# Kernel optimization log

Hardware: AMD Instinct MI355X
Metric: run time of the kernel (lower is better)

Reference implementation:

```python
import jax, jax.numpy as jnp
import numpy as np


def _reduce1(x):
    # x: [B, n, d] -> [B, 2d]; exists=max, forall=min over objects (exclude_self is a no-op for cnt=1)
    return jnp.concatenate([x.max(axis=1), x.min(axis=1)], axis=-1)


def _reduce2(x):
    # x: [B, n, n, d] -> [B, n, 2d]; exclude_self masks diagonal i==j (0 for exists/max, 1 for forall/min)
    n = x.shape[1]
    diag = jnp.eye(n, dtype=bool)[None, :, :, None]
    exists = jnp.where(diag, 0.0, x).max(axis=2)
    forall = jnp.where(diag, 1.0, x).min(axis=2)
    return jnp.concatenate([exists, forall], axis=-1)


def _layer(f0, f1, f2, p):
    # One LogicLayer step (breadth=2, minmax reducer, exclude_self, sigmoid norm, no hidden layers)
    W0, b0, W1, b1, W2, b2 = p
    B, n, d1 = f1.shape
    # order 0: [self, reduce(order1)]
    g0 = jnp.concatenate([f0, _reduce1(f1)], axis=-1)
    o0 = jax.nn.sigmoid(g0 @ W0 + b0)
    # order 1: [expand(order0), self, reduce(order2)]
    e0 = jnp.broadcast_to(f0[:, None, :], (B, n, f0.shape[-1]))
    g1 = jnp.concatenate([e0, f1, _reduce2(f2)], axis=-1)
    o1 = jax.nn.sigmoid(g1 @ W1 + b1)
    # order 2: [expand(order1), self] then Permutation(2) = cat(x, swap(i,j))
    e1 = jnp.broadcast_to(f1[:, :, None, :], (B, n, n, d1))
    g2 = jnp.concatenate([e1, f2], axis=-1)
    g2 = jnp.concatenate([g2, jnp.swapaxes(g2, 1, 2)], axis=-1)
    o2 = jax.nn.sigmoid(g2 @ W2 + b2)
    return o0, o1, o2


def setup_inputs() -> dict:
    key = jax.random.key(0)
    B, n = 4, 256
    d = [32, 64, 64]
    O = 128
    ks = iter(jax.random.split(key, 64))
    inp = {
        "x0": jax.random.uniform(next(ks), (B, d[0]), dtype=jnp.float32),
        "x1": jax.random.uniform(next(ks), (B, n, d[1]), dtype=jnp.float32),
        "x2": jax.random.uniform(next(ks), (B, n, n, d[2]), dtype=jnp.float32),
    }
    fan_ins = [
        (d[0] + 2 * d[1], d[0] + d[1] + 2 * d[2], 2 * (d[1] + d[2])),  # layer 0
        (O + 2 * O, O + O + 2 * O, 2 * (O + O)),                        # layer 1
        (O + 2 * O, O + O + 2 * O, 2 * (O + O)),                        # layer 2
    ]
    for l, fins in enumerate(fan_ins):
        for o, fin in enumerate(fins):
            inp[f"W{o}_{l}"] = jax.random.normal(next(ks), (fin, O), dtype=jnp.float32) / np.sqrt(fin).astype(np.float32)
            inp[f"b{o}_{l}"] = jnp.zeros((O,), dtype=jnp.float32)
    return inp


def reference(x0, x1, x2,
              W0_0, b0_0, W1_0, b1_0, W2_0, b2_0,
              W0_1, b0_1, W1_1, b1_1, W2_1, b2_1,
              W0_2, b0_2, W1_2, b1_2, W2_2, b2_2):
    f = (x0, x1, x2)
    for p in ((W0_0, b0_0, W1_0, b1_0, W2_0, b2_0),
              (W0_1, b0_1, W1_1, b1_1, W2_1, b2_1),
              (W0_2, b0_2, W1_2, b1_2, W2_2, b2_2)):
        f = _layer(*f, p)
    return f
```

## Files before the change

kernel.cpp:

```cpp
#include <hip/hip_runtime.h>
#include <hip/hip_bf16.h>
#include <cstdint>

#define NN 256
#define NB 4
#define OC 128

using bf16x8_t = __attribute__((ext_vector_type(8))) __bf16;
using f32x4_t  = __attribute__((ext_vector_type(4))) float;

typedef const __attribute__((address_space(1))) uint8_t* gptr1_t;
typedef __attribute__((address_space(3))) uint8_t* lptr3_t;

__device__ __forceinline__ void async_load16(const void* g, void* l) {
  __builtin_amdgcn_global_load_lds((gptr1_t)g, (lptr3_t)l, 16, 0, 0);
}

__device__ __forceinline__ float sigf(float x) {
  return __builtin_amdgcn_rcpf(1.0f + __expf(-x));
}

__device__ __forceinline__ uint16_t f2bf_rne(float f) {
  uint32_t u = __float_as_uint(f);
  uint32_t r = (u + 0x7fffu + ((u >> 16) & 1u)) >> 16;
  return (uint16_t)r;
}

__device__ __forceinline__ void emit_wt(const float* __restrict__ W2,
                                        uint16_t* __restrict__ Wt, int d1,
                                        int d2, int idx) {
  const int K = 2 * d2;
  const int nn = idx / K, k = idx - nn * K;
  const int row = (k < d2) ? (d1 + k) : (2 * d1 + d2 + (k - d2));
  Wt[idx] = f2bf_rne(W2[row * OC + nn]);
}

__device__ __forceinline__ void emit_bt(const float* __restrict__ W1,
                                        const float* __restrict__ W2,
                                        uint16_t* __restrict__ Bt, int D0,
                                        int D1, int D2, int FIN1, int KP,
                                        int idx) {
  const int n = idx / KP, k = idx - n * KP;
  float val = 0.f;
  if (n < 128) {
    if (k < FIN1) val = W1[k * OC + n];
  } else if (n < 256) {
    if (k >= D0 && k < D0 + D1) val = W2[(k - D0) * OC + (n - 128)];
  } else {
    if (k >= D0 && k < D0 + D1) val = W2[(D1 + D2 + (k - D0)) * OC + (n - 256)];
  }
  Bt[idx] = f2bf_rne(val);
}

__global__ __launch_bounds__(256) void prep_reduce(
    const float* __restrict__ W2_0, const float* __restrict__ W2_1,
    const float* __restrict__ W2_2, const float* __restrict__ W1_0,
    const float* __restrict__ W1_1, const float* __restrict__ W1_2,
    const float* __restrict__ x0, const float* __restrict__ x1,
    uint16_t* __restrict__ Wt0, uint16_t* __restrict__ Wt1,
    uint16_t* __restrict__ Wt2, uint16_t* __restrict__ Bt0,
    uint16_t* __restrict__ Bt1, uint16_t* __restrict__ Bt2,
    uint16_t* __restrict__ g1bf0, float* __restrict__ r2b,
    float* __restrict__ r2c, const float* __restrict__ x2,
    uint16_t* __restrict__ x2bf) {
  __shared__ float4 smx[256], smn[256];
  const int blk = blockIdx.x;
  const int tid = threadIdx.x;

  if (blk < 4800) {
    int g = blk * 256 + tid;
    if (g < 16384) { emit_wt(W2_0, Wt0, 64, 64, g); return; }
    g -= 16384;
    if (g < 32768) { emit_wt(W2_1, Wt1, 128, 128, g); return; }
    g -= 32768;
    if (g < 32768) { emit_wt(W2_2, Wt2, 128, 128, g); return; }
    g -= 32768;
    if (g < 98304) { emit_bt(W1_0, W2_0, Bt0, 32, 64, 64, 224, 256, g); return; }
    g -= 98304;
    if (g < 196608) { emit_bt(W1_1, W2_1, Bt1, 128, 128, 128, 512, 512, g); return; }
    g -= 196608;
    if (g < 196608) { emit_bt(W1_2, W2_2, Bt2, 128, 128, 128, 512, 512, g); return; }
    g -= 196608;
    if (g < 131072) {
      const int row = g >> 7, t = g & 127;
      uint16_t* const gp = g1bf0 + (size_t)row * 256;
      if (t < 32) gp[t] = f2bf_rne(x0[(row >> 8) * 32 + t]);
      else if (t < 96) gp[t] = f2bf_rne(x1[(size_t)row * 64 + (t - 32)]);
      else gp[128 + t] = 0;
      return;
    }
    g -= 131072;
    if (g < 262144) { r2b[g] = ((g & 255) < 128) ? 0.f : 1.f; return; }
    g -= 262144;
    if (g < 262144) { r2c[g] = ((g & 255) < 128) ? 0.f : 1.f; }
    return;
  }

  const int bid = blk - 4800;
  const int i = bid & 255;
  const int q = tid & 15, s = tid >> 4;
  const size_t rowbase = ((size_t)bid * NN) * 64 + q * 4;
  float mxA0 = 0.f, mxA1 = 0.f, mxA2 = 0.f, mxA3 = 0.f;
  float mnA0 = 1.f, mnA1 = 1.f, mnA2 = 1.f, mnA3 = 1.f;
  float mxB0 = 0.f, mxB1 = 0.f, mxB2 = 0.f, mxB3 = 0.f;
  float mnB0 = 1.f, mnB1 = 1.f, mnB2 = 1.f, mnB3 = 1.f;
#pragma unroll 2
  for (int t = 0; t < 16; t += 2) {
    const int jA = s + t * 16, jB = jA + 16;
    const float4 xa = *(const float4*)(x2 + rowbase + (size_t)jA * 64);
    const float4 xb = *(const float4*)(x2 + rowbase + (size_t)jB * 64);
    uint2 pa, pb;
    pa.x = (uint32_t)f2bf_rne(xa.x) | ((uint32_t)f2bf_rne(xa.y) << 16);
    pa.y = (uint32_t)f2bf_rne(xa.z) | ((uint32_t)f2bf_rne(xa.w) << 16);
    pb.x = (uint32_t)f2bf_rne(xb.x) | ((uint32_t)f2bf_rne(xb.y) << 16);
    pb.y = (uint32_t)f2bf_rne(xb.z) | ((uint32_t)f2bf_rne(xb.w) << 16);
    *(uint2*)(x2bf + rowbase + (size_t)jA * 64) = pa;
    *(uint2*)(x2bf + rowbase + (size_t)jB * 64) = pb;
    if (jA != i) {
      mxA0 = fmaxf(mxA0, xa.x); mxA1 = fmaxf(mxA1, xa.y);
      mxA2 = fmaxf(mxA2, xa.z); mxA3 = fmaxf(mxA3, xa.w);
      mnA0 = fminf(mnA0, xa.x); mnA1 = fminf(mnA1, xa.y);
      mnA2 = fminf(mnA2, xa.z); mnA3 = fminf(mnA3, xa.w);
    }
    if (jB != i) {
      mxB0 = fmaxf(mxB0, xb.x); mxB1 = fmaxf(mxB1, xb.y);
      mxB2 = fmaxf(mxB2, xb.z); mxB3 = fmaxf(mxB3, xb.w);
      mnB0 = fminf(mnB0, xb.x); mnB1 = fminf(mnB1, xb.y);
      mnB2 = fminf(mnB2, xb.z); mnB3 = fminf(mnB3, xb.w);
    }
  }
  float mx0 = fmaxf(mxA0, mxB0), mx1 = fmaxf(mxA1, mxB1);
  float mx2 = fmaxf(mxA2, mxB2), mx3 = fmaxf(mxA3, mxB3);
  float mn0 = fminf(mnA0, mnB0), mn1 = fminf(mnA1, mnB1);
  float mn2 = fminf(mnA2, mnB2), mn3 = fminf(mnA3, mnB3);
  smx[tid] = make_float4(mx0, mx1, mx2, mx3);
  smn[tid] = make_float4(mn0, mn1, mn2, mn3);
  __syncthreads();
  if (s == 0) {
    for (int ss = 1; ss < 16; ++ss) {
      float4 a = smx[q + ss * 16], c = smn[q + ss * 16];
      mx0 = fmaxf(mx0, a.x); mx1 = fmaxf(mx1, a.y);
      mx2 = fmaxf(mx2, a.z); mx3 = fmaxf(mx3, a.w);
      mn0 = fminf(mn0, c.x); mn1 = fminf(mn1, c.y);
      mn2 = fminf(mn2, c.z); mn3 = fminf(mn3, c.w);
    }
    uint16_t* const g = g1bf0 + (size_t)bid * 256;
    g[96 + q * 4 + 0] = f2bf_rne(mx0); g[96 + q * 4 + 1] = f2bf_rne(mx1);
    g[96 + q * 4 + 2] = f2bf_rne(mx2); g[96 + q * 4 + 3] = f2bf_rne(mx3);
    g[160 + q * 4 + 0] = f2bf_rne(mn0); g[160 + q * 4 + 1] = f2bf_rne(mn1);
    g[160 + q * 4 + 2] = f2bf_rne(mn2); g[160 + q * 4 + 3] = f2bf_rne(mn3);
  }
}

template <int KP, int D0, int D1, bool DUP, bool R2FUSE>
__global__ __launch_bounds__(256) void small_gemm(
    const uint16_t* __restrict__ g1, const uint16_t* __restrict__ Bt,
    const float* __restrict__ b1, const float* __restrict__ b2,
    float* __restrict__ f1out, uint16_t* __restrict__ g1next,
    float* __restrict__ u, float* __restrict__ vT,
    const float* __restrict__ f0in, const float* __restrict__ f1in,
    const float* __restrict__ W0, const float* __restrict__ b0,
    float* __restrict__ f0out, const float* __restrict__ r2src) {
  constexpr int NCH = KP / 64;
  const int bid = blockIdx.x;
  const int tid = threadIdx.x;

  __shared__ __align__(16) uint8_t ldsA[8192];
  __shared__ __align__(16) uint8_t ldsB[16384];

  if (bid < 48) {
    const int mt = bid / 3, nt = bid - mt * 3;
    const int m0 = mt * 64, n0 = nt * 128;
    const int wv = tid >> 6, lane = tid & 63;
    const int l15 = lane & 15, l4 = lane >> 4;

    f32x4_t acc[4][2];
#pragma unroll
    for (int a = 0; a < 4; ++a)
#pragma unroll
      for (int q = 0; q < 2; ++q) acc[a][q] = (f32x4_t){0.f, 0.f, 0.f, 0.f};

    for (int c = 0; c < NCH; ++c) {
      const int kbg = c * 64;
#pragma unroll
      for (int t = 0; t < 2; ++t) {
        const int id = wv * 2 + t;
        const int mi = id & 3, ks = id >> 2;
        if (R2FUSE && kbg >= KP / 2) {
          const float* const src = r2src +
              (size_t)(m0 + mi * 16 + l15) * (KP / 2) + (kbg - KP / 2) +
              ks * 32 + l4 * 8;
          const float4 fa = *(const float4*)(src);
          const float4 fb = *(const float4*)(src + 4);
          uint4 v;
          v.x = (uint32_t)f2bf_rne(fa.x) | ((uint32_t)f2bf_rne(fa.y) << 16);
          v.y = (uint32_t)f2bf_rne(fa.z) | ((uint32_t)f2bf_rne(fa.w) << 16);
          v.z = (uint32_t)f2bf_rne(fb.x) | ((uint32_t)f2bf_rne(fb.y) << 16);
          v.w = (uint32_t)f2bf_rne(fb.z) | ((uint32_t)f2bf_rne(fb.w) << 16);
          *(uint4*)(ldsA + id * 1024 + (lane << 4)) = v;
        } else {
          async_load16(
              g1 + (size_t)(m0 + mi * 16 + l15) * KP + kbg + ks * 32 + l4 * 8,
              ldsA + id * 1024);
        }
      }
#pragma unroll
      for (int t = 0; t < 4; ++t) {
        const int id = wv * 4 + t;
        const int ni = id & 7, ks = id >> 3;
        async_load16(Bt + (size_t)(n0 + ni * 16 + l15) * KP + kbg + ks * 32 + l4 * 8,
                     ldsB + id * 1024);
      }
      __syncthreads();
#pragma unroll
      for (int ks = 0; ks < 2; ++ks) {
        bf16x8_t Af[4], Bf[2];
#pragma unroll
        for (int a = 0; a < 4; ++a)
          Af[a] = *(const bf16x8_t*)(ldsA + ((ks * 4 + a) << 10) + (lane << 4));
#pragma unroll
        for (int q = 0; q < 2; ++q)
          Bf[q] = *(const bf16x8_t*)(ldsB + ((ks * 8 + wv * 2 + q) << 10) + (lane << 4));
#pragma unroll
        for (int a = 0; a < 4; ++a)
#pragma unroll
          for (int q = 0; q < 2; ++q)
            acc[a][q] = __builtin_amdgcn_mfma_f32_16x16x32_bf16(Af[a], Bf[q],
                                                                acc[a][q], 0, 0, 0);
      }
      __syncthreads();
    }

    float bias[2];
#pragma unroll
    for (int q = 0; q < 2; ++q) {
      const int cc = wv * 32 + q * 16 + l15;
      bias[q] = (nt == 0) ? b1[cc] : ((nt == 1) ? b2[cc] : 0.f);
    }
#pragma unroll
    for (int a = 0; a < 4; ++a) {
      const int rl = a * 16 + l4 * 4;
#pragma unroll
      for (int r = 0; r < 4; ++r) {
        const size_t bi = m0 + rl + r;
#pragma unroll
        for (int q = 0; q < 2; ++q) {
          const int cc = wv * 32 + q * 16 + l15;
          const float x = acc[a][q][r] + bias[q];
          if (nt == 0) {
            const float val = sigf(x);
            f1out[bi * OC + cc] = val;
            if (DUP) g1next[bi * 512 + 128 + cc] = f2bf_rne(val);
          } else if (nt == 1) {
            u[bi * OC + cc] = x;
          } else {
            const int b = (int)(bi >> 8), j = (int)(bi & 255);
            vT[((size_t)b * OC + cc) * NN + j] = x;
          }
        }
      }
    }
  } else {
    constexpr int FIN0 = D0 + 2 * D1;
    constexpr int S = 256 / D1;
    const int b = bid - 48;
    float* const sm = (float*)ldsA;
    float* const g0 = sm;
    float* const smx = sm + 512;
    float* const smn = sm + 768;
    float* const sval = sm + 1024;
    const int cc = tid & (D1 - 1), ss = tid / D1;
    float mx = -1e30f, mn = 1e30f;
    const float* f1b = f1in + (size_t)b * NN * D1;
    for (int j = ss; j < NN; j += S) {
      const float x = f1b[(size_t)j * D1 + cc];
      mx = fmaxf(mx, x); mn = fminf(mn, x);
    }
    smx[tid] = mx; smn[tid] = mn;
    __syncthreads();
    if (ss == 0) {
      for (int s2 = 1; s2 < S; ++s2) {
        mx = fmaxf(mx, smx[cc + s2 * D1]);
        mn = fminf(mn, smn[cc + s2 * D1]);
      }
      g0[D0 + cc] = mx;
      g0[D0 + D1 + cc] = mn;
    }
    if (tid < D0) g0[tid] = f0in[b * D0 + tid];
    __syncthreads();
    if (tid < OC) {
      float acc = b0[tid];
#pragma unroll 8
      for (int k = 0; k < FIN0; ++k) acc += g0[k] * W0[k * OC + tid];
      const float val = sigf(acc);
      f0out[b * OC + tid] = val;
      sval[tid] = val;
    }
    if (DUP) {
      __syncthreads();
      for (int idx = tid; idx < 256 * 128; idx += 256) {
        const int row = idx >> 7, c2 = idx & 127;
        g1next[((size_t)(b * 256 + row)) * 512 + c2] = f2bf_rne(sval[c2]);
      }
    }
  }
}

template <int D2, typename OUT_T, bool REDUCE>
__global__ __launch_bounds__(256, 4) void gemm2_kernel(
    const __hip_bfloat16* __restrict__ f2, const uint16_t* __restrict__ Wt,
    const float* __restrict__ u, const float* __restrict__ vT,
    OUT_T* __restrict__ out, float* __restrict__ r2n) {
  constexpr int K = 2 * D2;
  constexpr int NCH = K / 32;
  constexpr bool BF16OUT = (sizeof(OUT_T) == 2);
  constexpr int LDSB = BF16OUT ? (128 * 272) : 32768;
  const int bid = blockIdx.x;
  const int jt = bid & 1, i = (bid >> 1) & 255, b = bid >> 9;
  const int j0 = jt * 128;
  const int tid = threadIdx.x;
  const int wv = tid >> 6, lane = tid & 63;
  const int wr = wv >> 1, wc = wv & 1;
  const int l15 = lane & 15, l4 = lane >> 4;

  __shared__ __align__(16) uint8_t lds[LDSB];
  __shared__ unsigned smax[128], smin[128];

  const __hip_bfloat16* const A1 = f2 + ((size_t)(b * NN + i) * NN + j0) * D2;
  const __hip_bfloat16* const A2 = f2 + ((size_t)(b * NN + j0) * NN + i) * D2;

  f32x4_t acc[4][4];
#pragma unroll
  for (int a = 0; a < 4; ++a)
#pragma unroll
    for (int q = 0; q < 4; ++q) acc[a][q] = (f32x4_t){0.f, 0.f, 0.f, 0.f};

  auto STAGE = [&](int c, int buf) {
    const int kbg = c * 32;
    uint8_t* const bA = lds + buf * 16384;
    uint8_t* const bW = bA + 8192;
    const bool second = (kbg >= D2);
    const __hip_bfloat16* const Ab = second ? A2 : A1;
    const size_t rstride = second ? (size_t)NN * D2 : (size_t)D2;
    const int kbase = second ? (kbg - D2) : kbg;
#pragma unroll
    for (int t = 0; t < 2; ++t) {
      const int mi = wv * 2 + t;
      async_load16(Ab + (size_t)(mi * 16 + l15) * rstride + kbase + l4 * 8,
                   bA + mi * 1024);
    }
#pragma unroll
    for (int t = 0; t < 2; ++t) {
      const int ni = wv * 2 + t;
      async_load16(Wt + (size_t)(ni * 16 + l15) * K + kbg + l4 * 8,
                   bW + ni * 1024);
    }
  };

  auto COMPUTE = [&](int buf) {
    const uint8_t* const bA = lds + buf * 16384;
    const uint8_t* const bW = bA + 8192;
    bf16x8_t Af[4], Bf[4];
#pragma unroll
    for (int a = 0; a < 4; ++a)
      Af[a] = *(const bf16x8_t*)(bA + ((wr * 4 + a) << 10) + (lane << 4));
#pragma unroll
    for (int q = 0; q < 4; ++q)
      Bf[q] = *(const bf16x8_t*)(bW + ((wc * 4 + q) << 10) + (lane << 4));
#pragma unroll
    for (int a = 0; a < 4; ++a)
#pragma unroll
      for (int q = 0; q < 4; ++q)
        acc[a][q] = __builtin_amdgcn_mfma_f32_16x16x32_bf16(Af[a], Bf[q],
                                                            acc[a][q], 0, 0, 0);
  };

  STAGE(0, 0);
#pragma unroll
  for (int c = 0; c < NCH - 1; ++c) {
    STAGE(c + 1, (c + 1) & 1);
    asm volatile("s_waitcnt vmcnt(4)" ::: "memory");
    __builtin_amdgcn_sched_barrier(0);
    __builtin_amdgcn_s_barrier();
    __builtin_amdgcn_sched_barrier(0);
    COMPUTE(c & 1);
    asm volatile("s_waitcnt lgkmcnt(0)" ::: "memory");
    __builtin_amdgcn_sched_barrier(0);
    __builtin_amdgcn_s_barrier();
    __builtin_amdgcn_sched_barrier(0);
  }
  asm volatile("s_waitcnt vmcnt(0)" ::: "memory");
  __builtin_amdgcn_sched_barrier(0);
  __builtin_amdgcn_s_barrier();
  __builtin_amdgcn_sched_barrier(0);
  COMPUTE((NCH - 1) & 1);
  __syncthreads();

  const size_t bi2 = (size_t)(b * NN + i);
  float uval[4];
#pragma unroll
  for (int q = 0; q < 4; ++q) uval[q] = u[bi2 * OC + wc * 64 + q * 16 + l15];
  const size_t obase = (bi2 * NN + j0) * OC;
  const float* const vTb = vT + (size_t)b * OC * NN;

  if (BF16OUT) {
    if (REDUCE && tid < 128) { smax[tid] = 0u; smin[tid] = 0x3f800000u; }
    __syncthreads();
    float lmx[4] = {0.f, 0.f, 0.f, 0.f};
    float lmn[4] = {1.f, 1.f, 1.f, 1.f};
#pragma unroll
    for (int a = 0; a < 4; ++a) {
      const int rowb = wr * 64 + a * 16 + l4 * 4;
      const int jg = j0 + rowb;
#pragma unroll
      for (int q = 0; q < 4; ++q) {
        const int col = wc * 64 + q * 16 + l15;
        const float4 vq = *(const float4*)(vTb + (size_t)col * NN + jg);
#pragma unroll
        for (int r = 0; r < 4; ++r) {
          const int j = rowb + r;
          const float x = acc[a][q][r] + uval[q] + ((const float*)&vq)[r];
          const float sg = sigf(x);
          *(uint16_t*)(lds + j * 272 + col * 2) = f2bf_rne(sg);
          if (REDUCE && (jg + r) != i) {
            lmx[q] = fmaxf(lmx[q], sg);
            lmn[q] = fminf(lmn[q], sg);
          }
        }
      }
    }
    if (REDUCE) {
#pragma unroll
      for (int q = 0; q < 4; ++q) {
        const int col = wc * 64 + q * 16 + l15;
        atomicMax(&smax[col], __float_as_uint(lmx[q]));
        atomicMin(&smin[col], __float_as_uint(lmn[q]));
      }
    }
    __syncthreads();
    uint16_t* const outp = (uint16_t*)out;
#pragma unroll
    for (int ci = 0; ci < 8; ++ci) {
      const int chunk = ci * 256 + tid;
      const int row = chunk >> 4, off = chunk & 15;
      const uint4 val = *(const uint4*)(lds + row * 272 + off * 16);
      *(uint4*)(outp + obase + (size_t)row * OC + off * 8) = val;
    }
    if (REDUCE && tid < 128) {
      unsigned* const r2u = (unsigned*)r2n;
      atomicMax(&r2u[bi2 * 256 + tid], smax[tid]);
      atomicMin(&r2u[bi2 * 256 + 128 + tid], smin[tid]);
    }
  } else {
    float* const outp = (float*)out;
#pragma unroll
    for (int a = 0; a < 4; ++a) {
      const int rowb = wr * 64 + a * 16 + l4 * 4;
      const int jg = j0 + rowb;
#pragma unroll
      for (int q = 0; q < 4; ++q) {
        const int col = wc * 64 + q * 16 + l15;
        const float4 vq = *(const float4*)(vTb + (size_t)col * NN + jg);
#pragma unroll
        for (int r = 0; r < 4; ++r) {
          const int j = rowb + r;
          const float x = acc[a][q][r] + uval[q] + ((const float*)&vq)[r];
          outp[obase + (size_t)j * OC + col] = sigf(x);
        }
      }
    }
  }
}

extern "C" void kernel_launch(void* const* d_in, const int* in_sizes, int n_in,
                              void* d_out, int out_size, void* d_ws,
                              size_t ws_size, hipStream_t stream) {
  const float* x0 = (const float*)d_in[0];
  const float* x1 = (const float*)d_in[1];
  const float* x2 = (const float*)d_in[2];
  const float *Wp[3][3], *bp[3][3];
  for (int l = 0; l < 3; ++l)
    for (int o = 0; o < 3; ++o) {
      Wp[l][o] = (const float*)d_in[3 + l * 6 + o * 2];
      bp[l][o] = (const float*)d_in[3 + l * 6 + o * 2 + 1];
    }

  const size_t F2E = (size_t)NB * NN * NN * OC;
  const size_t X2E = (size_t)NB * NN * NN * 64;

  uint8_t* ws = (uint8_t*)d_ws;
  size_t off = 0;
  auto carve = [&](size_t bytes) -> uint8_t* {
    uint8_t* p = ws + off;
    off += (bytes + 255) & ~(size_t)255;
    return p;
  };
  float* f0a = (float*)carve((size_t)NB * OC * 4);
  float* f0b = (float*)carve((size_t)NB * OC * 4);
  float* f1a = (float*)carve((size_t)NB * NN * OC * 4);
  float* f1b = (float*)carve((size_t)NB * NN * OC * 4);
  float* r2b = (float*)carve((size_t)NB * NN * 256 * 4);
  float* r2c = (float*)carve((size_t)NB * NN * 256 * 4);
  float* uu  = (float*)carve((size_t)NB * NN * OC * 4);
  float* vT  = (float*)carve((size_t)NB * OC * NN * 4);
  uint16_t* Wt0 = (uint16_t*)carve((size_t)OC * 128 * 2);
  uint16_t* Wt1 = (uint16_t*)carve((size_t)OC * 256 * 2);
  uint16_t* Wt2 = (uint16_t*)carve((size_t)OC * 256 * 2);
  uint16_t* Bt0 = (uint16_t*)carve((size_t)384 * 256 * 2);
  uint16_t* Bt1 = (uint16_t*)carve((size_t)384 * 512 * 2);
  uint16_t* Bt2 = (uint16_t*)carve((size_t)384 * 512 * 2);
  uint16_t* g1bf0 = (uint16_t*)carve((size_t)NB * NN * 256 * 2);
  uint16_t* g1bf1 = (uint16_t*)carve((size_t)NB * NN * 512 * 2);
  uint16_t* g1bf2 = (uint16_t*)carve((size_t)NB * NN * 512 * 2);
  __hip_bfloat16* f2a = (__hip_bfloat16*)carve(F2E * 2);

  __hip_bfloat16* f2b;
  uint16_t* x2bf;
  if (ws_size >= off + F2E * 2) {
    f2b = (__hip_bfloat16*)carve(F2E * 2);
    x2bf = (uint16_t*)f2b;
  } else {
    f2b = (__hip_bfloat16*)d_in[2];
    x2bf = (uint16_t*)carve(X2E * 2);
  }

  float* out_f0 = (float*)d_out;
  float* out_f1 = out_f0 + (size_t)NB * OC;
  float* out_f2 = out_f1 + (size_t)NB * NN * OC;

  prep_reduce<<<4800 + NB * NN, 256, 0, stream>>>(
      Wp[0][2], Wp[1][2], Wp[2][2], Wp[0][1], Wp[1][1], Wp[2][1], x0, x1, Wt0,
      Wt1, Wt2, Bt0, Bt1, Bt2, g1bf0, r2b, r2c, x2, x2bf);

  small_gemm<256, 32, 64, true, false><<<52, 256, 0, stream>>>(
      g1bf0, Bt0, bp[0][1], bp[0][2], f1a, g1bf1, uu, vT, x0, x1, Wp[0][0],
      bp[0][0], f0a, nullptr);
  gemm2_kernel<64, __hip_bfloat16, true><<<NB * NN * 2, 256, 0, stream>>>(
      (const __hip_bfloat16*)x2bf, Wt0, uu, vT, f2a, r2b);

  small_gemm<512, 128, 128, true, true><<<52, 256, 0, stream>>>(
      g1bf1, Bt1, bp[1][1], bp[1][2], f1b, g1bf2, uu, vT, f0a, f1a, Wp[1][0],
      bp[1][0], f0b, r2b);
  gemm2_kernel<128, __hip_bfloat16, true><<<NB * NN * 2, 256, 0, stream>>>(
      f2a, Wt1, uu, vT, f2b, r2c);

  small_gemm<512, 128, 128, false, true><<<52, 256, 0, stream>>>(
      g1bf2, Bt2, bp[2][1], bp[2][2], out_f1, nullptr, uu, vT, f0b, f1b,
      Wp[2][0], bp[2][0], out_f0, r2c);
  gemm2_kernel<128, float, false><<<NB * NN * 2, 256, 0, stream>>>(
      f2b, Wt2, uu, vT, out_f2, nullptr);
}
```

Measured before the change: 513.4 us.

## Fuse all stages into a persistent megakernel with grid barriers and overlap

Replaces the seven kernel launches (prep/reduce, three small GEMMs, three pairwise GEMMs) with one persistent kernel of 1024 blocks. Stages are separated by a software grid barrier built on atomic counters. Within each layer, the 52 small-GEMM blocks publish a done counter, and the other blocks run the pairwise GEMM main loop straight away. They only wait on that counter before the epilogue that needs u/vT. This removes launch gaps and lets the small per-layer GEMM overlap the large GEMM. The cost is barrier and fence overhead, and the design relies on all 1024 blocks being co-resident (4 per CU); if they are not, the grid barrier deadlocks.

```diff
diff --git a/kernel.cpp b/kernel.cpp
--- a/kernel.cpp
+++ b/kernel.cpp
@@ -5,6 +5,7 @@
 #define NN 256
 #define NB 4
 #define OC 128
+#define GRID 1024
 
 using bf16x8_t = __attribute__((ext_vector_type(8))) __bf16;
 using f32x4_t  = __attribute__((ext_vector_type(4))) float;
@@ -24,6 +25,49 @@
   uint32_t u = __float_as_uint(f);
   uint32_t r = (u + 0x7fffu + ((u >> 16) & 1u)) >> 16;
   return (uint16_t)r;
+}
+
+struct Ctrs { unsigned ctr, gen, done0, done1, done2; };
+
+__device__ __forceinline__ void gbar(Ctrs* C, int tid) {
+  __syncthreads();
+  if (tid == 0) {
+    __threadfence();
+    unsigned g = __hip_atomic_load(&C->gen, __ATOMIC_RELAXED,
+                                   __HIP_MEMORY_SCOPE_AGENT);
+    unsigned a = __hip_atomic_fetch_add(&C->ctr, 1u, __ATOMIC_ACQ_REL,
+                                        __HIP_MEMORY_SCOPE_AGENT);
+    if (a == GRID - 1) {
+      __hip_atomic_store(&C->ctr, 0u, __ATOMIC_RELAXED,
+                         __HIP_MEMORY_SCOPE_AGENT);
+      __hip_atomic_fetch_add(&C->gen, 1u, __ATOMIC_RELEASE,
+                             __HIP_MEMORY_SCOPE_AGENT);
+    } else {
+      while (__hip_atomic_load(&C->gen, __ATOMIC_ACQUIRE,
+                               __HIP_MEMORY_SCOPE_AGENT) == g)
+        __builtin_amdgcn_s_sleep(8);
+    }
+    __threadfence();
+  }
+  __syncthreads();
+  __builtin_amdgcn_fence(__ATOMIC_ACQUIRE, "agent");
+}
+
+__device__ __forceinline__ void mark_done(unsigned* d, int tid) {
+  __syncthreads();
+  __builtin_amdgcn_fence(__ATOMIC_RELEASE, "agent");
+  if (tid == 0)
+    __hip_atomic_fetch_add(d, 1u, __ATOMIC_RELAXED, __HIP_MEMORY_SCOPE_AGENT);
+}
+
+__device__ __forceinline__ void wait_done(unsigned* d, int tid) {
+  if (tid == 0) {
+    while (__hip_atomic_load(d, __ATOMIC_RELAXED, __HIP_MEMORY_SCOPE_AGENT) <
+           52u)
+      __builtin_amdgcn_s_sleep(8);
+  }
+  __syncthreads();
+  __builtin_amdgcn_fence(__ATOMIC_ACQUIRE, "agent");
 }
 
 __device__ __forceinline__ void emit_wt(const float* __restrict__ W2,
@@ -52,51 +96,44 @@
   Bt[idx] = f2bf_rne(val);
 }
 
-__global__ __launch_bounds__(256) void prep_reduce(
-    const float* __restrict__ W2_0, const float* __restrict__ W2_1,
-    const float* __restrict__ W2_2, const float* __restrict__ W1_0,
-    const float* __restrict__ W1_1, const float* __restrict__ W1_2,
-    const float* __restrict__ x0, const float* __restrict__ x1,
-    uint16_t* __restrict__ Wt0, uint16_t* __restrict__ Wt1,
-    uint16_t* __restrict__ Wt2, uint16_t* __restrict__ Bt0,
-    uint16_t* __restrict__ Bt1, uint16_t* __restrict__ Bt2,
-    uint16_t* __restrict__ g1bf0, float* __restrict__ r2b,
-    float* __restrict__ r2c, const float* __restrict__ x2,
-    uint16_t* __restrict__ x2bf) {
-  __shared__ float4 smx[256], smn[256];
-  const int blk = blockIdx.x;
-  const int tid = threadIdx.x;
-
-  if (blk < 4800) {
-    int g = blk * 256 + tid;
-    if (g < 16384) { emit_wt(W2_0, Wt0, 64, 64, g); return; }
-    g -= 16384;
-    if (g < 32768) { emit_wt(W2_1, Wt1, 128, 128, g); return; }
-    g -= 32768;
-    if (g < 32768) { emit_wt(W2_2, Wt2, 128, 128, g); return; }
-    g -= 32768;
-    if (g < 98304) { emit_bt(W1_0, W2_0, Bt0, 32, 64, 64, 224, 256, g); return; }
-    g -= 98304;
-    if (g < 196608) { emit_bt(W1_1, W2_1, Bt1, 128, 128, 128, 512, 512, g); return; }
-    g -= 196608;
-    if (g < 196608) { emit_bt(W1_2, W2_2, Bt2, 128, 128, 128, 512, 512, g); return; }
-    g -= 196608;
-    if (g < 131072) {
-      const int row = g >> 7, t = g & 127;
-      uint16_t* const gp = g1bf0 + (size_t)row * 256;
-      if (t < 32) gp[t] = f2bf_rne(x0[(row >> 8) * 32 + t]);
-      else if (t < 96) gp[t] = f2bf_rne(x1[(size_t)row * 64 + (t - 32)]);
-      else gp[128 + t] = 0;
-      return;
-    }
-    g -= 131072;
-    if (g < 262144) { r2b[g] = ((g & 255) < 128) ? 0.f : 1.f; return; }
-    g -= 262144;
-    if (g < 262144) { r2c[g] = ((g & 255) < 128) ? 0.f : 1.f; }
+__device__ void prep_unit(
+    int g, const float* W2_0, const float* W2_1, const float* W2_2,
+    const float* W1_0, const float* W1_1, const float* W1_2, const float* x0,
+    const float* x1, uint16_t* Wt0, uint16_t* Wt1, uint16_t* Wt2,
+    uint16_t* Bt0, uint16_t* Bt1, uint16_t* Bt2, uint16_t* g1bf0, float* r2b,
+    float* r2c) {
+  if (g < 16384) { emit_wt(W2_0, Wt0, 64, 64, g); return; }
+  g -= 16384;
+  if (g < 32768) { emit_wt(W2_1, Wt1, 128, 128, g); return; }
+  g -= 32768;
+  if (g < 32768) { emit_wt(W2_2, Wt2, 128, 128, g); return; }
+  g -= 32768;
+  if (g < 98304) { emit_bt(W1_0, W2_0, Bt0, 32, 64, 64, 224, 256, g); return; }
+  g -= 98304;
+  if (g < 196608) { emit_bt(W1_1, W2_1, Bt1, 128, 128, 128, 512, 512, g); return; }
+  g -= 196608;
+  if (g < 196608) { emit_bt(W1_2, W2_2, Bt2, 128, 128, 128, 512, 512, g); return; }
+  g -= 196608;
+  if (g < 131072) {
+    const int row = g >> 7, t = g & 127;
+    uint16_t* const gp = g1bf0 + (size_t)row * 256;
+    if (t < 32) gp[t] = f2bf_rne(x0[(row >> 8) * 32 + t]);
+    else if (t < 96) gp[t] = f2bf_rne(x1[(size_t)row * 64 + (t - 32)]);
+    else gp[128 + t] = 0;
     return;
   }
-
-  const int bid = blk - 4800;
+  g -= 131072;
+  if (g < 262144) { r2b[g] = ((g & 255) < 128) ? 0.f : 1.f; return; }
+  g -= 262144;
+  if (g < 262144) { r2c[g] = ((g & 255) < 128) ? 0.f : 1.f; }
+}
+
+__device__ void reduce2_unit(int bid, const float* __restrict__ x2,
+                             uint16_t* __restrict__ g1bf0,
+                             uint16_t* __restrict__ x2bf, uint8_t* ldsraw,
+                             int tid) {
+  float4* const smx = (float4*)ldsraw;
+  float4* const smn = (float4*)(ldsraw + 4096);
   const int i = bid & 255;
   const int q = tid & 15, s = tid >> 4;
   const size_t rowbase = ((size_t)bid * NN) * 64 + q * 4;
@@ -153,21 +190,19 @@
 }
 
 template <int KP, int D0, int D1, bool DUP, bool R2FUSE>
-__global__ __launch_bounds__(256) void small_gemm(
-    const uint16_t* __restrict__ g1, const uint16_t* __restrict__ Bt,
-    const float* __restrict__ b1, const float* __restrict__ b2,
-    float* __restrict__ f1out, uint16_t* __restrict__ g1next,
-    float* __restrict__ u, float* __restrict__ vT,
-    const float* __restrict__ f0in, const float* __restrict__ f1in,
-    const float* __restrict__ W0, const float* __restrict__ b0,
-    float* __restrict__ f0out, const float* __restrict__ r2src) {
+__device__ void sg_body(int bid, const uint16_t* __restrict__ g1,
+                        const uint16_t* __restrict__ Bt,
+                        const float* __restrict__ b1,
+                        const float* __restrict__ b2, float* __restrict__ f1out,
+                        uint16_t* __restrict__ g1next, float* __restrict__ u,
+                        float* __restrict__ vT, const float* __restrict__ f0in,
+                        const float* __restrict__ f1in,
+                        const float* __restrict__ W0,
+                        const float* __restrict__ b0,
+                        float* __restrict__ f0out,
+                        const float* __restrict__ r2src, uint8_t* ldsA,
+                        uint8_t* ldsB, int tid) {
   constexpr int NCH = KP / 64;
-  const int bid = blockIdx.x;
-  const int tid = threadIdx.x;
-
-  __shared__ __align__(16) uint8_t ldsA[8192];
-  __shared__ __align__(16) uint8_t ldsB[16384];
-
   if (bid < 48) {
     const int mt = bid / 3, nt = bid - mt * 3;
     const int m0 = mt * 64, n0 = nt * 128;
@@ -307,24 +342,23 @@
 }
 
 template <int D2, typename OUT_T, bool REDUCE>
-__global__ __launch_bounds__(256, 4) void gemm2_kernel(
-    const __hip_bfloat16* __restrict__ f2, const uint16_t* __restrict__ Wt,
-    const float* __restrict__ u, const float* __restrict__ vT,
-    OUT_T* __restrict__ out, float* __restrict__ r2n) {
+__device__ void gemm2_body(int tile, const __hip_bfloat16* __restrict__ f2,
+                           const uint16_t* __restrict__ Wt,
+                           const float* __restrict__ u,
+                           const float* __restrict__ vT,
+                           OUT_T* __restrict__ out, float* __restrict__ r2n,
+                           unsigned* done, uint8_t* lds, unsigned* smax,
+                           unsigned* smin, int tid) {
   constexpr int K = 2 * D2;
   constexpr int NCH = K / 32;
   constexpr bool BF16OUT = (sizeof(OUT_T) == 2);
-  constexpr int LDSB = BF16OUT ? (128 * 272) : 32768;
-  const int bid = blockIdx.x;
-  const int jt = bid & 1, i = (bid >> 1) & 255, b = bid >> 9;
+  const int jt = tile & 1, i = (tile >> 1) & 255, b = tile >> 9;
   const int j0 = jt * 128;
-  const int tid = threadIdx.x;
   const int wv = tid >> 6, lane = tid & 63;
   const int wr = wv >> 1, wc = wv & 1;
   const int l15 = lane & 15, l4 = lane >> 4;
 
-  __shared__ __align__(16) uint8_t lds[LDSB];
-  __shared__ unsigned smax[128], smin[128];
+  __syncthreads();
 
   const __hip_bfloat16* const A1 = f2 + ((size_t)(b * NN + i) * NN + j0) * D2;
   const __hip_bfloat16* const A2 = f2 + ((size_t)(b * NN + j0) * NN + i) * D2;
@@ -396,6 +430,8 @@
   COMPUTE((NCH - 1) & 1);
   __syncthreads();
 
+  wait_done(done, tid);
+
   const size_t bi2 = (size_t)(b * NN + i);
   float uval[4];
 #pragma unroll
@@ -470,6 +506,73 @@
       }
     }
   }
+}
+
+__global__ __launch_bounds__(256, 4) void megakernel(
+    Ctrs* C, const float* x0, const float* x1, const float* x2,
+    const float* W0_0, const float* b0_0, const float* W1_0, const float* b1_0,
+    const float* W2_0, const float* b2_0, const float* W0_1, const float* b0_1,
+    const float* W1_1, const float* b1_1, const float* W2_1, const float* b2_1,
+    const float* W0_2, const float* b0_2, const float* W1_2, const float* b1_2,
+    const float* W2_2, const float* b2_2, uint16_t* Wt0, uint16_t* Wt1,
+    uint16_t* Wt2, uint16_t* Bt0, uint16_t* Bt1, uint16_t* Bt2,
+    uint16_t* g1bf0, uint16_t* g1bf1, uint16_t* g1bf2, float* r2b, float* r2c,
+    float* f0a, float* f0b, float* f1a, float* f1b, float* uu, float* vT,
+    uint16_t* x2bf, __hip_bfloat16* f2a, __hip_bfloat16* f2b, float* out_f0,
+    float* out_f1, float* out_f2) {
+  __shared__ __align__(16) uint8_t lds[34816];
+  __shared__ unsigned smax[128], smin[128];
+  const int bid = blockIdx.x;
+  const int tid = threadIdx.x;
+
+  for (int p = 0; p < 6; ++p) {
+    const int unit = p * GRID + bid;
+    if (unit < 4800) {
+      prep_unit(unit * 256 + tid, W2_0, W2_1, W2_2, W1_0, W1_1, W1_2, x0, x1,
+                Wt0, Wt1, Wt2, Bt0, Bt1, Bt2, g1bf0, r2b, r2c);
+    } else if (unit < 5824) {
+      reduce2_unit(unit - 4800, x2, g1bf0, x2bf, lds, tid);
+    }
+    __syncthreads();
+  }
+  gbar(C, tid);
+
+  if (bid < 52) {
+    sg_body<256, 32, 64, true, false>(bid, g1bf0, Bt0, b1_0, b2_0, f1a, g1bf1,
+                                      uu, vT, x0, x1, W0_0, b0_0, f0a, nullptr,
+                                      lds, lds + 8192, tid);
+    mark_done(&C->done0, tid);
+  }
+  gemm2_body<64, __hip_bfloat16, true>(bid, (const __hip_bfloat16*)x2bf, Wt0,
+                                       uu, vT, f2a, r2b, &C->done0, lds, smax,
+                                       smin, tid);
+  gemm2_body<64, __hip_bfloat16, true>(bid + GRID, (const __hip_bfloat16*)x2bf,
+                                       Wt0, uu, vT, f2a, r2b, &C->done0, lds,
+                                       smax, smin, tid);
+  gbar(C, tid);
+
+  if (bid < 52) {
+    sg_body<512, 128, 128, true, true>(bid, g1bf1, Bt1, b1_1, b2_1, f1b, g1bf2,
+                                       uu, vT, f0a, f1a, W0_1, b0_1, f0b, r2b,
+                                       lds, lds + 8192, tid);
+    mark_done(&C->done1, tid);
+  }
+  gemm2_body<128, __hip_bfloat16, true>(bid, f2a, Wt1, uu, vT, f2b, r2c,
+                                        &C->done1, lds, smax, smin, tid);
+  gemm2_body<128, __hip_bfloat16, true>(bid + GRID, f2a, Wt1, uu, vT, f2b, r2c,
+                                        &C->done1, lds, smax, smin, tid);
+  gbar(C, tid);
+
+  if (bid < 52) {
+    sg_body<512, 128, 128, false, true>(bid, g1bf2, Bt2, b1_2, b2_2, out_f1,
+                                        nullptr, uu, vT, f0b, f1b, W0_2, b0_2,
+                                        out_f0, r2c, lds, lds + 8192, tid);
+    mark_done(&C->done2, tid);
+  }
+  gemm2_body<128, float, false>(bid, f2b, Wt2, uu, vT, out_f2, nullptr,
+                                &C->done2, lds, smax, smin, tid);
+  gemm2_body<128, float, false>(bid + GRID, f2b, Wt2, uu, vT, out_f2, nullptr,
+                                &C->done2, lds, smax, smin, tid);
 }
 
 extern "C" void kernel_launch(void* const* d_in, const int* in_sizes, int n_in,
@@ -495,6 +598,7 @@
     off += (bytes + 255) & ~(size_t)255;
     return p;
   };
+  Ctrs* ctrs = (Ctrs*)carve(256);
   float* f0a = (float*)carve((size_t)NB * OC * 4);
   float* f0b = (float*)carve((size_t)NB * OC * 4);
   float* f1a = (float*)carve((size_t)NB * NN * OC * 4);
@@ -528,25 +632,11 @@
   float* out_f1 = out_f0 + (size_t)NB * OC;
   float* out_f2 = out_f1 + (size_t)NB * NN * OC;
 
-  prep_reduce<<<4800 + NB * NN, 256, 0, stream>>>(
-      Wp[0][2], Wp[1][2], Wp[2][2], Wp[0][1], Wp[1][1], Wp[2][1], x0, x1, Wt0,
-      Wt1, Wt2, Bt0, Bt1, Bt2, g1bf0, r2b, r2c, x2, x2bf);
-
-  small_gemm<256, 32, 64, true, false><<<52, 256, 0, stream>>>(
-      g1bf0, Bt0, bp[0][1], bp[0][2], f1a, g1bf1, uu, vT, x0, x1, Wp[0][0],
-      bp[0][0], f0a, nullptr);
-  gemm2_kernel<64, __hip_bfloat16, true><<<NB * NN * 2, 256, 0, stream>>>(
-      (const __hip_bfloat16*)x2bf, Wt0, uu, vT, f2a, r2b);
-
-  small_gemm<512, 128, 128, true, true><<<52, 256, 0, stream>>>(
-      g1bf1, Bt1, bp[1][1], bp[1][2], f1b, g1bf2, uu, vT, f0a, f1a, Wp[1][0],
-      bp[1][0], f0b, r2b);
-  gemm2_kernel<128, __hip_bfloat16, true><<<NB * NN * 2, 256, 0, stream>>>(
-      f2a, Wt1, uu, vT, f2b, r2c);
-
-  small_gemm<512, 128, 128, false, true><<<52, 256, 0, stream>>>(
-      g1bf2, Bt2, bp[2][1], bp[2][2], out_f1, nullptr, uu, vT, f0b, f1b,
-      Wp[2][0], bp[2][0], out_f0, r2c);
-  gemm2_kernel<128, float, false><<<NB * NN * 2, 256, 0, stream>>>(
-      f2b, Wt2, uu, vT, out_f2, nullptr);
-}
+  hipMemsetAsync(ctrs, 0, sizeof(Ctrs), stream);
+  megakernel<<<GRID, 256, 0, stream>>>(
+      ctrs, x0, x1, x2, Wp[0][0], bp[0][0], Wp[0][1], bp[0][1], Wp[0][2],
+      bp[0][2], Wp[1][0], bp[1][0], Wp[1][1], bp[1][1], Wp[1][2], bp[1][2],
+      Wp[2][0], bp[2][0], Wp[2][1], bp[2][1], Wp[2][2], bp[2][2], Wt0, Wt1,
+      Wt2, Bt0, Bt1, Bt2, g1bf0, g1bf1, g1bf2, r2b, r2c, f0a, f0b, f1a, f1b,
+      uu, vT, x2bf, f2a, f2b, out_f0, out_f1, out_f2);
+}
```

After: 1.537 ms. +199.4%, slower.
